# Optimization experiments

Measured on AMD Instinct MI355X. Metric: run time of the kernel, lower is better.

The kernel has to match this reference:

```python
import jax, jax.numpy as jnp
import numpy as np

SEQ, BATCH, IN, HID, LAYERS, TAPE = 256, 128, 512, 512, 2, 30


def setup_inputs() -> dict:
    key = jax.random.key(0)
    ks = jax.random.split(key, 10)
    s = 0.05  # small init scale for numerical stability of tanh/softmax
    return {
        "xs": jax.random.normal(ks[0], (SEQ, BATCH, IN), jnp.float32),
        # stacked per-layer LSTM params (layer-1 input dim == HID == IN)
        "W_ih": jax.random.normal(ks[1], (LAYERS, 4 * HID, IN), jnp.float32) * s,
        "W_hh": jax.random.normal(ks[2], (LAYERS, 4 * HID, HID), jnp.float32) * s,
        "b_ih": jax.random.normal(ks[3], (LAYERS, 4 * HID), jnp.float32) * s,
        "b_hh": jax.random.normal(ks[4], (LAYERS, 4 * HID), jnp.float32) * s,
        "attn_wh": jax.random.normal(ks[5], (LAYERS, HID, HID), jnp.float32) * s,
        "attn_wx": jax.random.normal(ks[6], (LAYERS, HID, IN), jnp.float32) * s,
        "attn_wht": jax.random.normal(ks[7], (LAYERS, HID, HID), jnp.float32) * s,
        "attn_v": jax.random.normal(ks[8], (LAYERS, HID), jnp.float32) * s,
    }


def reference(xs, W_ih, W_hh, b_ih, b_hh, attn_wh, attn_wx, attn_wht, attn_v):
    L, B, H = W_ih.shape[0], xs.shape[1], W_hh.shape[-1]

    def lstm_step(x, h, c):
        # x: (B, IN); h, c: (L, B, H). PyTorch gate order: i, f, g, o.
        inp = x
        hs, cs = [], []
        for l in range(L):
            gates = inp @ W_ih[l].T + b_ih[l] + h[l] @ W_hh[l].T + b_hh[l]
            i_, f_, g_, o_ = jnp.split(gates, 4, axis=-1)
            c_new = jax.nn.sigmoid(f_) * c[l] + jax.nn.sigmoid(i_) * jnp.tanh(g_)
            h_new = jax.nn.sigmoid(o_) * jnp.tanh(c_new)
            hs.append(h_new)
            cs.append(c_new)
            inp = h_new
        return jnp.stack(hs), jnp.stack(cs)

    zeros = jnp.zeros((L, B, H), xs.dtype)
    # First TAPE steps: source never updates prev_hidden/cell inside the fill
    # loop, so every step starts from zero state -> vmap over time.
    h_tape0, c_tape0 = jax.vmap(lambda x: lstm_step(x, zeros, zeros))(xs[:TAPE])

    # einsums 'jll,...' / 'ijj,...' contract nothing: they take diagonals.
    wh_diag = jnp.diagonal(attn_wh, axis1=1, axis2=2)    # (L, H)
    wht_diag = jnp.diagonal(attn_wht, axis1=1, axis2=2)  # (L, H)

    def step(carry, x):
        h_tape, c_tape, prev_h = carry
        hidden_attn = h_tape * wh_diag[:, None, :]            # (T, L, B, H)
        x_attn = jnp.einsum('lhi,bi->lbh', attn_wx, x)        # (L, B, H)
        ht_attn = prev_h * wht_diag[:, None, :]               # (L, B, H)
        a = jnp.tanh(hidden_attn + x_attn + ht_attn)          # (T, L, B, H)
        score = jnp.einsum('tlbh,lh->tlb', a, attn_v)         # (T, L, B)
        alpha = jax.nn.softmax(score, axis=0)
        prev_h_new = jnp.einsum('tlb,tlbh->lbh', alpha, h_tape)
        prev_c_new = jnp.einsum('tlb,tlbh->lbh', alpha, c_tape)
        h_new, c_new = lstm_step(x, prev_h_new, prev_c_new)
        h_tape = jnp.concatenate([h_tape[1:], h_new[None]], axis=0)
        c_tape = jnp.concatenate([c_tape[1:], c_new[None]], axis=0)
        return (h_tape, c_tape, prev_h_new), None

    (h_tape, _, _), _ = jax.lax.scan(step, (h_tape0, c_tape0, zeros), xs[TAPE:])
    return h_tape[:, -1]  # (TAPE, B, H): last layer across the tape
```

## Files before the change

### kernel.cpp

```cpp
#include <hip/hip_runtime.h>
#include <hip/hip_fp16.h>

typedef _Float16 f16;
typedef _Float16 half8 __attribute__((ext_vector_type(8)));
typedef _Float16 half4v __attribute__((ext_vector_type(4)));
typedef float floatx4 __attribute__((ext_vector_type(4)));
typedef unsigned long long u64;

#define SEQ   256
#define BATCH 128
#define HID   512
#define NL    2
#define TAPE  30
#define NG    2048
#define NBLK  256

__device__ __forceinline__ float fsig(float x)  { return 1.f/(1.f+__expf(-x)); }
__device__ __forceinline__ float ftanh(float x) { return 1.f - 2.f/(1.f+__expf(2.f*x)); }

__device__ __forceinline__ void ast64(void* p, u64 v){
    __hip_atomic_store((u64*)p, v, __ATOMIC_RELAXED, __HIP_MEMORY_SCOPE_AGENT);
}
__device__ __forceinline__ void ast32(void* p, unsigned v){
    __hip_atomic_store((unsigned*)p, v, __ATOMIC_RELAXED, __HIP_MEMORY_SCOPE_AGENT);
}
__device__ __forceinline__ unsigned packh2(float a, float b){
    union { f16 h[2]; unsigned u; } c; c.h[0]=(f16)a; c.h[1]=(f16)b; return c.u;
}
__device__ __forceinline__ float2 unpackh2(unsigned u){
    union { unsigned u; f16 h[2]; } c; c.u=u;
    float2 r; r.x=(float)c.h[0]; r.y=(float)c.h[1]; return r;
}

#define BAR_ROOT 512
#define BAR_REL  544
__device__ __forceinline__ void gridbar(unsigned* bar, unsigned gen){
    __syncthreads();
    if (threadIdx.x == 0){
        unsigned* leaf = bar + ((blockIdx.x >> 4) << 5);
        bool releaser = false;
        unsigned p = __hip_atomic_fetch_add(leaf, 1u, __ATOMIC_RELAXED, __HIP_MEMORY_SCOPE_AGENT);
        if ((p & 15u) == 15u){
            unsigned q = __hip_atomic_fetch_add(bar + BAR_ROOT, 1u, __ATOMIC_RELAXED, __HIP_MEMORY_SCOPE_AGENT);
            if ((q & 15u) == 15u){
                __hip_atomic_store(bar + BAR_REL, gen, __ATOMIC_RELAXED, __HIP_MEMORY_SCOPE_AGENT);
                releaser = true;
            }
        }
        if (!releaser){
            while (__hip_atomic_load(bar + BAR_REL, __ATOMIC_RELAXED, __HIP_MEMORY_SCOPE_AGENT) < gen){
                __builtin_amdgcn_s_sleep(8);
            }
        }
        __builtin_amdgcn_fence(__ATOMIC_ACQUIRE, "agent");
    }
    __syncthreads();
}

__global__ void k_setup_w(const float* __restrict__ W_ih, const float* __restrict__ W_hh,
                          const float* __restrict__ b_ih, const float* __restrict__ b_hh,
                          f16* __restrict__ Wcat, float* __restrict__ bsum)
{
    int idx = blockIdx.x*256 + threadIdx.x;
    int l = idx >> 21;
    int r = (idx >> 10) & 2047;
    int k = idx & 1023;
    int gate = r & 3, h = r >> 2;
    int orig = gate*HID + h;
    float wv = (k < 512) ? W_ih[((size_t)l*NG + orig)*512 + k]
                         : W_hh[((size_t)l*NG + orig)*512 + (k-512)];
    Wcat[idx] = (f16)wv;
    if (idx < NL*NG) {
        int l2 = idx >> 11, r2 = idx & 2047;
        int g2 = r2 & 3, h2 = r2 >> 2;
        int o2 = g2*HID + h2;
        bsum[idx] = b_ih[l2*NG + o2] + b_hh[l2*NG + o2];
    }
}

__global__ void k_setup_misc(const float* __restrict__ attn_wx, const float* __restrict__ attn_wh,
                             const float* __restrict__ attn_wht, const float* __restrict__ attn_v,
                             f16* __restrict__ awx, float* __restrict__ whd,
                             float* __restrict__ whtd, float* __restrict__ av)
{
    int idx = blockIdx.x*256 + threadIdx.x;
    awx[idx] = (f16)attn_wx[idx];
    if (idx < NL*HID) {
        int l = idx >> 9, h = idx & 511;
        whd[idx]  = attn_wh[((size_t)l*HID + h)*HID + h];
        whtd[idx] = attn_wht[((size_t)l*HID + h)*HID + h];
        av[idx]   = attn_v[idx];
    }
}

__global__ void k_xs16(const float* __restrict__ x, f16* __restrict__ o)
{
    size_t i = ((size_t)blockIdx.x*256 + threadIdx.x)*4;
    float4 v = *(const float4*)(x + i);
    half4v h; h[0]=(f16)v.x; h[1]=(f16)v.y; h[2]=(f16)v.z; h[3]=(f16)v.w;
    *(half4v*)(o + i) = h;
}

#define MFMA4(af, bf) do { \
    acc[0][0] = __builtin_amdgcn_mfma_f32_16x16x32_f16(af[0], bf[0], acc[0][0], 0, 0, 0); \
    acc[0][1] = __builtin_amdgcn_mfma_f32_16x16x32_f16(af[0], bf[1], acc[0][1], 0, 0, 0); \
    acc[1][0] = __builtin_amdgcn_mfma_f32_16x16x32_f16(af[1], bf[0], acc[1][0], 0, 0, 0); \
    acc[1][1] = __builtin_amdgcn_mfma_f32_16x16x32_f16(af[1], bf[1], acc[1][1], 0, 0, 0); \
} while(0)

__global__ __launch_bounds__(512) void k_xattn(const f16* __restrict__ Xf,
                                               const f16* __restrict__ AWX,
                                               f16* __restrict__ XA)
{
    int nb = blockIdx.x;
    int t  = blockIdx.y;
    int l  = blockIdx.z;
    const f16* A  = Xf  + (size_t)t*(BATCH*512);
    const f16* Bm = AWX + (size_t)l*(512*512);
    int lane = threadIdx.x & 63, wid = threadIdx.x >> 6;
    int wm = wid >> 1, wn = wid & 1;
    int row0 = wm*32 + (lane & 15);
    int col0 = nb*64 + wn*32 + (lane & 15);
    int kc = (lane >> 4)*8;
    const f16* a_base = A  + row0*512 + kc;
    const f16* b_base = Bm + col0*512 + kc;
    floatx4 acc[2][2] = {};
    #pragma unroll 4
    for (int ks = 0; ks < 16; ks++){
        half8 af[2], bf[2];
        af[0] = *(const half8*)(a_base + ks*32);
        af[1] = *(const half8*)(a_base + 8192 + ks*32);
        bf[0] = *(const half8*)(b_base + ks*32);
        bf[1] = *(const half8*)(b_base + 8192 + ks*32);
        MFMA4(af, bf);
    }
    int rr = (lane >> 4)*4;
    #pragma unroll
    for (int mi = 0; mi < 2; mi++)
    #pragma unroll
    for (int ni = 0; ni < 2; ni++)
    #pragma unroll
    for (int j = 0; j < 4; j++){
        int brow = wm*32 + mi*16 + rr + j;
        int ch   = nb*64 + wn*32 + ni*16 + (lane & 15);
        XA[(((size_t)t*NL + l)*BATCH + brow)*HID + ch] = (f16)acc[mi][ni][j];
    }
}

__global__ __launch_bounds__(512) void k_fill(const f16* __restrict__ A0all,
                                              const f16* __restrict__ B,
                                              const float* __restrict__ bsum_l,
                                              f16* __restrict__ htape16, float* __restrict__ ctape,
                                              int l, f16* __restrict__ h0out)
{
    int y  = blockIdx.y;
    int nb = blockIdx.x;
    const f16* A0 = A0all + (size_t)y*(BATCH*HID);
    if (h0out) h0out += (size_t)y*(BATCH*HID);

    int tid = threadIdx.x, lane = tid & 63, wid = tid >> 6;
    int wm = wid >> 1, wn = wid & 1;
    int row0 = wm*32 + (lane & 15);
    int col0 = nb*64 + wn*32 + (lane & 15);
    int kc = (lane >> 4)*8;
    const f16* a_base = A0 + row0*512 + kc;
    const f16* b_base = B + (size_t)col0*1024 + kc;

    floatx4 acc[2][2] = {};
    #pragma unroll
    for (int ks = 0; ks < 16; ks++){
        half8 af[2], bf[2];
        af[0] = *(const half8*)(a_base + ks*32);
        af[1] = *(const half8*)(a_base + 16*512 + ks*32);
        bf[0] = *(const half8*)(b_base + ks*32);
        bf[1] = *(const half8*)(b_base + (size_t)16*1024 + ks*32);
        MFMA4(af, bf);
    }

    __shared__ float Cl[128][65];
    int rr = (lane >> 4)*4;
    #pragma unroll
    for (int mi = 0; mi < 2; mi++)
    #pragma unroll
    for (int ni = 0; ni < 2; ni++){
        float bias = bsum_l[col0 + ni*16];
        #pragma unroll
        for (int j = 0; j < 4; j++)
            Cl[wm*32 + mi*16 + rr + j][wn*32 + ni*16 + (lane & 15)] = acc[mi][ni][j] + bias;
    }
    __syncthreads();

    #pragma unroll
    for (int it = 0; it < 4; it++){
        int item = tid + it*512;
        int b = item >> 4, hl = item & 15;
        float gi = Cl[b][hl*4+0];
        float gg = Cl[b][hl*4+2];
        float go = Cl[b][hl*4+3];
        int hg = nb*16 + hl;
        float cn = fsig(gi)*ftanh(gg);
        float hn = fsig(go)*ftanh(cn);
        size_t toff = (((size_t)y*NL + l)*BATCH + b)*HID + hg;
        htape16[toff] = (f16)hn;
        ctape[toff]   = cn;
        if (h0out) h0out[b*HID + hg] = (f16)hn;
    }
}

struct SArgs {
    const f16* xsf; const f16* xattn; const f16* Wcat; const float* bsum;
    const float* whd; const float* whtd; const float* av;
    const f16* htape16; const float* ctape;
    float* prevc; f16* prevh16;
    f16* h016; float2* slotstage; float* out;
    unsigned* bar;
};

__global__ __launch_bounds__(256, 1) void k_scan(SArgs A)
{
    __shared__ f16 Wsh[16*1024];
    __shared__ float2 stg[128*4];
    __shared__ float wpart[TAPE][4];
    __shared__ unsigned ringH[TAPE][256];
    __shared__ unsigned ringC[TAPE][256];

    const int blk = blockIdx.x;
    const int tid = threadIdx.x;
    const int lane = tid & 63, wv = tid >> 6;
    const int myl = blk >> 7;
    const int cb  = blk & 127;
    const int b   = blk & 127;
    const int h0  = tid*2;
    const size_t BH = (size_t)BATCH*HID;

    {
        const f16* src = A.Wcat + ((size_t)myl*NG + (size_t)cb*16)*1024;
        for (int i = tid; i < 2048; i += 256){
            int c = i >> 7;
            int k = (i & 127)*8;
            int dst = (c << 10) | (k ^ ((c & 7) << 3));
            *(half8*)&Wsh[dst] = *(const half8*)(src + ((size_t)c << 10) + k);
        }
    }

    float phx = 0.f, phy = 0.f;
    #pragma unroll
    for (int p = 0; p < TAPE; p++){
        size_t off = (((size_t)p*NL + myl)*BATCH + b)*HID + h0;
        ringH[p][tid] = *(const unsigned*)(A.htape16 + off);
        float2 cc = *(const float2*)(A.ctape + off);
        ringC[p][tid] = packh2(cc.x, cc.y);
    }
    __syncthreads();

    auto do_attn = [&](int t, bool consume){
        if (consume){
            int snew = (t-1) % TAPE;
            const float2* sl2 = A.slotstage + ((size_t)myl*BATCH + b)*HID + h0;
            float2 c0 = sl2[0], c1 = sl2[1];
            ringH[snew][tid] = packh2(c0.x, c1.x);
            ringC[snew][tid] = packh2(c0.y, c1.y);
        }
        size_t pb = ((size_t)myl*BATCH + b)*HID + h0;
        unsigned xu = *(const unsigned*)(A.xattn + (((size_t)t*NL + myl)*BATCH + b)*HID + h0);
        float2 xa = unpackh2(xu);
        int hw = myl*HID + h0;
        float wdx = A.whd[hw],  wdy = A.whd[hw+1];
        float wtx = A.whtd[hw], wty = A.whtd[hw+1];
        float vvx = A.av[hw],   vvy = A.av[hw+1];
        float bx = xa.x + phx*wtx, by = xa.y + phy*wty;

        float sc[TAPE];
        #pragma unroll
        for (int p = 0; p < TAPE; p++){
            float2 hv = unpackh2(ringH[p][tid]);
            float ax = ftanh(hv.x*wdx + bx);
            float ay = ftanh(hv.y*wdy + by);
            float s = ax*vvx + ay*vvy;
            #pragma unroll
            for (int o = 32; o; o >>= 1) s += __shfl_xor(s, o);
            if (lane == 0) wpart[p][wv] = s;
        }
        __syncthreads();
        float m = -1e30f;
        #pragma unroll
        for (int p = 0; p < TAPE; p++){
            sc[p] = wpart[p][0] + wpart[p][1] + wpart[p][2] + wpart[p][3];
            m = fmaxf(m, sc[p]);
        }
        float Z = 0.f;
        #pragma unroll
        for (int p = 0; p < TAPE; p++){ sc[p] = __expf(sc[p] - m); Z += sc[p]; }
        float inv = 1.f/Z;
        float ahx=0.f, ahy=0.f, acx=0.f, acy=0.f;
        #pragma unroll
        for (int p = 0; p < TAPE; p++){
            float2 hv = unpackh2(ringH[p][tid]);
            float2 cv = unpackh2(ringC[p][tid]);
            ahx += sc[p]*hv.x; ahy += sc[p]*hv.y;
            acx += sc[p]*cv.x; acy += sc[p]*cv.y;
        }
        ahx*=inv; ahy*=inv; acx*=inv; acy*=inv;
        phx = ahx; phy = ahy;
        ast32(A.prevh16 + pb, packh2(ahx, ahy));
        union { float2 f; u64 u; } pc; pc.f.x = acx; pc.f.y = acy;
        ast64(A.prevc + pb, pc.u);
    };

    auto do_gemm = [&](const f16* A0base, const f16* A1base,
                       f16* h0out, float* outp){
        int rowT = wv*32;
        int row0 = rowT + (lane & 15);
        int kc = (lane >> 4)*8;
        const f16* a0 = A0base + (size_t)row0*512 + kc;
        const f16* a1 = A1base + (size_t)row0*512 + kc;
        int colL = lane & 15;
        int bofs = colL << 10;
        int sw = (colL & 7) << 3;
        int rr = (lane >> 4) << 2;
        int hL = colL >> 2;
        int hG = cb*4 + hL;

        const float* cprev_l = A.prevc + (size_t)myl*BH;
        float cp[2][4];
        #pragma unroll
        for (int mi = 0; mi < 2; mi++)
        #pragma unroll
        for (int j = 0; j < 4; j++)
            cp[mi][j] = cprev_l[(size_t)(rowT + mi*16 + rr + j)*HID + hG];

        floatx4 acc0 = {0,0,0,0}, acc1 = {0,0,0,0};
        #pragma unroll
        for (int ks = 0; ks < 16; ks++){
            half8 af0 = *(const half8*)(a0 + ks*32);
            half8 af1 = *(const half8*)(a0 + ks*32 + 16*512);
            int kx = (kc + ks*32) ^ sw;
            half8 bf = *(const half8*)&Wsh[bofs + kx];
            acc0 = __builtin_amdgcn_mfma_f32_16x16x32_f16(af0, bf, acc0, 0, 0, 0);
            acc1 = __builtin_amdgcn_mfma_f32_16x16x32_f16(af1, bf, acc1, 0, 0, 0);
        }
        #pragma unroll
        for (int ks = 0; ks < 16; ks++){
            half8 af0 = *(const half8*)(a1 + ks*32);
            half8 af1 = *(const half8*)(a1 + ks*32 + 16*512);
            int kx = (kc + (ks+16)*32) ^ sw;
            half8 bf = *(const half8*)&Wsh[bofs + kx];
            acc0 = __builtin_amdgcn_mfma_f32_16x16x32_f16(af0, bf, acc0, 0, 0, 0);
            acc1 = __builtin_amdgcn_mfma_f32_16x16x32_f16(af1, bf, acc1, 0, 0, 0);
        }

        int baseLane = lane & 60;
        float bias = A.bsum[myl*NG + cb*16 + colL];
        #pragma unroll
        for (int mi = 0; mi < 2; mi++){
            #pragma unroll
            for (int j = 0; j < 4; j++){
                float g = (mi ? acc1[j] : acc0[j]) + bias;
                float gi = __shfl(g, baseLane+0);
                float gf = __shfl(g, baseLane+1);
                float gg = __shfl(g, baseLane+2);
                float go = __shfl(g, baseLane+3);
                int row = rowT + mi*16 + rr + j;
                float cn = fsig(gf)*cp[mi][j] + fsig(gi)*ftanh(gg);
                float hn = fsig(go)*ftanh(cn);
                if ((lane & 3) == 0){ float2 v; v.x=hn; v.y=cn; stg[row*4 + hL] = v; }
            }
        }
        __syncthreads();
        float2* slot2 = A.slotstage + (size_t)myl*BH;
        #pragma unroll
        for (int e = 0; e < 2; e++){
            int idx = tid + e*256;
            int row = idx >> 2, hh = idx & 3;
            union { float2 f; u64 u; } cu; cu.f = stg[idx];
            ast64(&slot2[(size_t)row*HID + cb*4 + hh], cu.u);
        }
        if (tid < 128){
            int row = tid;
            if (myl == 0){
                union { f16 h[4]; u64 u; } pk;
                pk.h[0]=(f16)stg[row*4+0].x; pk.h[1]=(f16)stg[row*4+1].x;
                pk.h[2]=(f16)stg[row*4+2].x; pk.h[3]=(f16)stg[row*4+3].x;
                ast64(h0out + (size_t)row*512 + cb*4, pk.u);
            } else {
                union { float2 f; u64 u; } p0, p1;
                p0.f.x = stg[row*4+0].x; p0.f.y = stg[row*4+1].x;
                p1.f.x = stg[row*4+2].x; p1.f.y = stg[row*4+3].x;
                ast64(outp + (size_t)row*512 + cb*4,     p0.u);
                ast64(outp + (size_t)row*512 + cb*4 + 2, p1.u);
            }
        }
    };

    if (myl == 0) do_attn(TAPE, false);
    unsigned gen = 0;
    gridbar(A.bar, ++gen);

    for (int t = TAPE; t < SEQ; ++t){
        if (myl == 0) do_gemm(A.xsf + (size_t)t*BH, A.prevh16, A.h016, nullptr);
        else          do_attn(t, t > TAPE);
        gridbar(A.bar, ++gen);
        if (myl == 1) do_gemm(A.h016, A.prevh16 + BH, nullptr,
                              A.out + (size_t)((t-16) % TAPE)*BH);
        else if (t + 1 < SEQ) do_attn(t + 1, true);
        gridbar(A.bar, ++gen);
    }
}

extern "C" void kernel_launch(void* const* d_in, const int* in_sizes, int n_in,
                              void* d_out, int out_size, void* d_ws, size_t ws_size,
                              hipStream_t stream)
{
    (void)in_sizes; (void)n_in; (void)out_size; (void)ws_size;
    const float* xs       = (const float*)d_in[0];
    const float* W_ih     = (const float*)d_in[1];
    const float* W_hh     = (const float*)d_in[2];
    const float* b_ih     = (const float*)d_in[3];
    const float* b_hh     = (const float*)d_in[4];
    const float* attn_wh  = (const float*)d_in[5];
    const float* attn_wx  = (const float*)d_in[6];
    const float* attn_wht = (const float*)d_in[7];
    const float* attn_v   = (const float*)d_in[8];
    float* out = (float*)d_out;

    char* w = (char*)d_ws;
    auto alloc = [&](size_t bytes)->char*{ char* p = w; w += (bytes + 255) & ~(size_t)255; return p; };
    f16*   Wcat    = (f16*)   alloc((size_t)NL*NG*1024*2);
    float* bsum    = (float*) alloc((size_t)NL*NG*4);
    f16*   awx     = (f16*)   alloc((size_t)NL*HID*HID*2);
    float* whd     = (float*) alloc((size_t)NL*HID*4);
    float* whtd    = (float*) alloc((size_t)NL*HID*4);
    float* av      = (float*) alloc((size_t)NL*HID*4);
    f16*   xsf     = (f16*)   alloc((size_t)SEQ*BATCH*HID*2);
    f16*   xattn   = (f16*)   alloc((size_t)SEQ*NL*BATCH*HID*2);
    f16*   htape16 = (f16*)   alloc((size_t)TAPE*NL*BATCH*HID*2);
    float* ctape   = (float*) alloc((size_t)TAPE*NL*BATCH*HID*4);
    float* prevc   = (float*) alloc((size_t)NL*BATCH*HID*4);
    f16*   prevh16 = (f16*)   alloc((size_t)NL*BATCH*HID*2);
    f16*   h016    = (f16*)   alloc((size_t)BATCH*HID*2);
    f16*   h0all   = (f16*)   alloc((size_t)TAPE*BATCH*HID*2);
    float2* slotstage = (float2*)alloc((size_t)NL*BATCH*HID*8);
    unsigned* bar  = (unsigned*)alloc(4096);

    hipMemsetAsync(prevc,   0, (size_t)NL*BATCH*HID*4, stream);
    hipMemsetAsync(prevh16, 0, (size_t)NL*BATCH*HID*2, stream);
    hipMemsetAsync(bar,     0, 4096, stream);

    k_setup_w   <<<dim3(16384), dim3(256), 0, stream>>>(W_ih, W_hh, b_ih, b_hh, Wcat, bsum);
    k_setup_misc<<<dim3(2048),  dim3(256), 0, stream>>>(attn_wx, attn_wh, attn_wht, attn_v, awx, whd, whtd, av);
    k_xs16      <<<dim3(16384), dim3(256), 0, stream>>>(xs, xsf);
    k_xattn     <<<dim3(8, SEQ, NL), dim3(512), 0, stream>>>(xsf, awx, xattn);

    k_fill<<<dim3(32, TAPE), dim3(512), 0, stream>>>(xsf, Wcat, bsum, htape16, ctape, 0, h0all);
    k_fill<<<dim3(32, TAPE), dim3(512), 0, stream>>>(h0all, Wcat + (size_t)NG*1024, bsum + NG,
                                                     htape16, ctape, 1, nullptr);

    SArgs sa;
    sa.xsf = xsf; sa.xattn = xattn; sa.Wcat = Wcat; sa.bsum = bsum;
    sa.whd = whd; sa.whtd = whtd; sa.av = av;
    sa.htape16 = htape16; sa.ctape = ctape;
    sa.prevc = prevc; sa.prevh16 = prevh16;
    sa.h016 = h016; sa.slotstage = slotstage; sa.out = out;
    sa.bar = bar;
    k_scan<<<dim3(NBLK), dim3(256), 0, stream>>>(sa);
}
```

Baseline: 7.405 ms.

## Split LSTM GEMM into input and recurrent halves to overlap with attention phase

The per-layer gate GEMM is split into an input-projection half and a recurrent half. The input half (x·W_ih or h0·W_ih) is computed in the phase before it is needed, alongside the attention work, so only the recurrent half and the gate activations stay on the critical path after each grid barrier. Layer 1's schedule shifts by one phase, and a tail step runs the final recurrent half after the loop. Accumulators now persist across barriers, which raises register pressure and makes the phase assignment harder to follow.

```diff
diff --git a/kernel.cpp b/kernel.cpp
--- a/kernel.cpp
+++ b/kernel.cpp
@@ -307,47 +307,38 @@
         ast64(A.prevc + pb, pc.u);
     };
 
-    auto do_gemm = [&](const f16* A0base, const f16* A1base,
-                       f16* h0out, float* outp){
-        int rowT = wv*32;
-        int row0 = rowT + (lane & 15);
-        int kc = (lane >> 4)*8;
-        const f16* a0 = A0base + (size_t)row0*512 + kc;
-        const f16* a1 = A1base + (size_t)row0*512 + kc;
-        int colL = lane & 15;
-        int bofs = colL << 10;
-        int sw = (colL & 7) << 3;
-        int rr = (lane >> 4) << 2;
-        int hL = colL >> 2;
-        int hG = cb*4 + hL;
-
-        const float* cprev_l = A.prevc + (size_t)myl*BH;
-        float cp[2][4];
-        #pragma unroll
-        for (int mi = 0; mi < 2; mi++)
-        #pragma unroll
-        for (int j = 0; j < 4; j++)
-            cp[mi][j] = cprev_l[(size_t)(rowT + mi*16 + rr + j)*HID + hG];
-
-        floatx4 acc0 = {0,0,0,0}, acc1 = {0,0,0,0};
+    floatx4 acc0 = {0,0,0,0}, acc1 = {0,0,0,0};
+    const int colL = lane & 15;
+    const int bofs = colL << 10;
+    const int sw   = (colL & 7) << 3;
+    const int rowT = wv*32;
+    const int row0g = rowT + (lane & 15);
+    const int kcl  = (lane >> 4)*8;
+    const int rr   = (lane >> 4) << 2;
+    const int hL   = colL >> 2;
+    const int hG   = cb*4 + hL;
+
+    auto gemm_half = [&](const f16* Abase, int kofs){
+        const f16* a = Abase + (size_t)row0g*512 + kcl;
         #pragma unroll
         for (int ks = 0; ks < 16; ks++){
-            half8 af0 = *(const half8*)(a0 + ks*32);
-            half8 af1 = *(const half8*)(a0 + ks*32 + 16*512);
-            int kx = (kc + ks*32) ^ sw;
+            half8 af0 = *(const half8*)(a + ks*32);
+            half8 af1 = *(const half8*)(a + ks*32 + 16*512);
+            int kx = (kcl + kofs + ks*32) ^ sw;
             half8 bf = *(const half8*)&Wsh[bofs + kx];
             acc0 = __builtin_amdgcn_mfma_f32_16x16x32_f16(af0, bf, acc0, 0, 0, 0);
             acc1 = __builtin_amdgcn_mfma_f32_16x16x32_f16(af1, bf, acc1, 0, 0, 0);
         }
-        #pragma unroll
-        for (int ks = 0; ks < 16; ks++){
-            half8 af0 = *(const half8*)(a1 + ks*32);
-            half8 af1 = *(const half8*)(a1 + ks*32 + 16*512);
-            int kx = (kc + (ks+16)*32) ^ sw;
-            half8 bf = *(const half8*)&Wsh[bofs + kx];
-            acc0 = __builtin_amdgcn_mfma_f32_16x16x32_f16(af0, bf, acc0, 0, 0, 0);
-            acc1 = __builtin_amdgcn_mfma_f32_16x16x32_f16(af1, bf, acc1, 0, 0, 0);
-        }
+    };
+
+    auto gemm_fin = [&](f16* h0out, float* outp){
+        const float* cprev_l = A.prevc + (size_t)myl*BH;
+        float cp[2][4];
+        #pragma unroll
+        for (int mi = 0; mi < 2; mi++)
+        #pragma unroll
+        for (int j = 0; j < 4; j++)
+            cp[mi][j] = cprev_l[(size_t)(rowT + mi*16 + rr + j)*HID + hG];
 
         int baseLane = lane & 60;
         float bias = A.bsum[myl*NG + cb*16 + colL];
@@ -390,20 +381,40 @@
                 ast64(outp + (size_t)row*512 + cb*4 + 2, p1.u);
             }
         }
+        floatx4 z = {0,0,0,0};
+        acc0 = z; acc1 = z;
     };
 
-    if (myl == 0) do_attn(TAPE, false);
+    if (myl == 0){
+        do_attn(TAPE, false);
+        gemm_half(A.xsf + (size_t)TAPE*BH, 0);
+    }
     unsigned gen = 0;
     gridbar(A.bar, ++gen);
 
     for (int t = TAPE; t < SEQ; ++t){
-        if (myl == 0) do_gemm(A.xsf + (size_t)t*BH, A.prevh16, A.h016, nullptr);
-        else          do_attn(t, t > TAPE);
+        if (myl == 0){
+            gemm_half(A.prevh16, 512);
+            gemm_fin(A.h016, nullptr);
+        } else if (t > TAPE){
+            gemm_half(A.prevh16 + BH, 512);
+            gemm_fin(nullptr, A.out + (size_t)((t-1-16) % TAPE)*BH);
+        }
         gridbar(A.bar, ++gen);
-        if (myl == 1) do_gemm(A.h016, A.prevh16 + BH, nullptr,
-                              A.out + (size_t)((t-16) % TAPE)*BH);
-        else if (t + 1 < SEQ) do_attn(t + 1, true);
+        if (myl == 0){
+            if (t + 1 < SEQ){
+                do_attn(t + 1, true);
+                gemm_half(A.xsf + (size_t)(t+1)*BH, 0);
+            }
+        } else {
+            do_attn(t, t > TAPE);
+            gemm_half(A.h016, 0);
+        }
         gridbar(A.bar, ++gen);
+    }
+    if (myl == 1){
+        gemm_half(A.prevh16 + BH, 512);
+        gemm_fin(nullptr, A.out + (size_t)((SEQ-1-16) % TAPE)*BH);
     }
 }
 
```

After: 7.354 ms. Within noise of the previous version (-0.7%).
